# Performance work log

Measured on AMD Instinct MI355X. Metric: run time of the kernel, lower is better.

Reference implementation:

```python
import jax, jax.numpy as jnp
import numpy as np

N, G, NPG = 51200, 512, 100
E, FA, FE = 300000, 64, 8
H, NH, DH, L, T = 256, 8, 32, 4, 5


def setup_inputs() -> dict:
    key = jax.random.key(0)
    it = iter(jax.random.split(key, 40))
    def rn(shape, s=0.05):
        return jax.random.normal(next(it), shape, jnp.float32) * s
    inp = {
        "x": rn((N, FA), 1.0),
        "edge_attr": rn((E, FE), 1.0),
        "edge_index": jax.random.randint(next(it), (2, E), 0, N),
        "batch": jnp.repeat(jnp.arange(G), NPG),
        "atom_w": rn((FA, H)), "atom_b": jnp.zeros((H,), jnp.float32),
        "edge_w": rn((FE, H)), "edge_b": jnp.zeros((H,), jnp.float32),
        "gat_lin_w": rn((L, H, H)), "gat_lin_edge_w": rn((L, H, H)),
        "gat_att_src": rn((L, NH, DH)), "gat_att_dst": rn((L, NH, DH)), "gat_att_edge": rn((L, NH, DH)),
        "gat_bias": jnp.zeros((L, H), jnp.float32),
        "bn_gamma": jnp.ones((L, H), jnp.float32), "bn_beta": jnp.zeros((L, H), jnp.float32),
        "mha_in_w": rn((3 * H, H)), "mha_in_b": jnp.zeros((3 * H,), jnp.float32),
        "mha_out_w": rn((H, H)), "mha_out_b": jnp.zeros((H,), jnp.float32),
        "sh_w1": rn((H, H)), "sh_b1": jnp.zeros((H,), jnp.float32),
        "sh_w2": rn((H, H // 2)), "sh_b2": jnp.zeros((H // 2,), jnp.float32),
        "head_w1": rn((T, H // 2, H // 4)), "head_b1": jnp.zeros((T, H // 4), jnp.float32),
        "head_w2": rn((T, H // 4, 1)), "head_b2": jnp.zeros((T, 1), jnp.float32),
    }
    return inp


def _forward(x, edge_attr, edge_index, batch, atom_w, atom_b, edge_w, edge_b,
             gat_lin_w, gat_lin_edge_w, gat_att_src, gat_att_dst, gat_att_edge,
             gat_bias, bn_gamma, bn_beta, mha_in_w, mha_in_b, mha_out_w, mha_out_b,
             sh_w1, sh_b1, sh_w2, sh_b2, head_w1, head_b1, head_w2, head_b2):
    src, dst = edge_index[0], edge_index[1]
    h = x @ atom_w + atom_b                      # [N, H] atom_encoder
    e = edge_attr @ edge_w + edge_b              # [E, H] edge_encoder
    # PyG GATConv add_self_loops=True, fill_value='mean' for edge_attr
    deg = jax.ops.segment_sum(jnp.ones((E,), e.dtype), dst, num_segments=N)
    e_self = jax.ops.segment_sum(e, dst, num_segments=N) / jnp.maximum(deg, 1.0)[:, None]
    loop = jnp.arange(N)
    src_f = jnp.concatenate([src, loop])
    dst_f = jnp.concatenate([dst, loop])
    e_f = jnp.concatenate([e, e_self], axis=0)   # [E+N, H]
    for i in range(L):
        res = h
        xs = (h @ gat_lin_w[i]).reshape(N, NH, DH)
        a_src = (xs * gat_att_src[i]).sum(-1)    # [N, NH]
        a_dst = (xs * gat_att_dst[i]).sum(-1)
        ee = (e_f @ gat_lin_edge_w[i]).reshape(-1, NH, DH)
        a_e = (ee * gat_att_edge[i]).sum(-1)     # [E+N, NH]
        alpha = jax.nn.leaky_relu(a_src[src_f] + a_dst[dst_f] + a_e, 0.2)
        mx = jax.ops.segment_max(alpha, dst_f, num_segments=N)   # segment softmax over dst
        ex = jnp.exp(alpha - mx[dst_f])
        den = jax.ops.segment_sum(ex, dst_f, num_segments=N)
        w = ex / (den[dst_f] + 1e-16)            # [E+N, NH]
        out = jax.ops.segment_sum(xs[src_f] * w[..., None], dst_f, num_segments=N)
        out = out.reshape(N, H) + gat_bias[i]
        mu = out.mean(0)
        var = out.var(0)                         # training-mode BatchNorm
        out = bn_gamma[i] * (out - mu) * jax.lax.rsqrt(var + 1e-5) + bn_beta[i]
        h = jax.nn.relu(out)
        if i > 0:
            h = h + res
    # per-graph MHA: graphs are fixed-size, so the ragged loop == batched attention
    xg = h.reshape(G, NPG, H)
    qkv = xg @ mha_in_w.T + mha_in_b             # [G, n, 3H]
    q, k, v = jnp.split(qkv, 3, axis=-1)
    def heads(t):
        return t.reshape(G, NPG, NH, DH).transpose(0, 2, 1, 3)
    q = heads(q) * (1.0 / np.sqrt(DH))
    k, v = heads(k), heads(v)
    att = jax.nn.softmax(jnp.einsum("ghnd,ghmd->ghnm", q, k), axis=-1)
    o = jnp.einsum("ghnm,ghmd->ghnd", att, v).transpose(0, 2, 1, 3).reshape(G, NPG, H)
    o = o @ mha_out_w.T + mha_out_b
    pooled = o.mean(1)                           # [G, H]
    s = jax.nn.relu(pooled @ sh_w1 + sh_b1)
    s = jax.nn.relu(s @ sh_w2 + sh_b2)           # [G, H//2]
    hh = jax.nn.relu(jnp.einsum("gd,tdk->gtk", s, head_w1) + head_b1)
    pred = jnp.einsum("gtk,tko->gto", hh, head_w2)[..., 0] + head_b2[:, 0]
    return pred                                  # [G, T]


def reference(x, edge_attr, edge_index, batch, atom_w, atom_b, edge_w, edge_b,
              gat_lin_w, gat_lin_edge_w, gat_att_src, gat_att_dst, gat_att_edge,
              gat_bias, bn_gamma, bn_beta, mha_in_w, mha_in_b, mha_out_w, mha_out_b,
              sh_w1, sh_b1, sh_w2, sh_b2, head_w1, head_b1, head_w2, head_b2):
    return _forward(x, edge_attr, edge_index, batch, atom_w, atom_b, edge_w, edge_b,
                    gat_lin_w, gat_lin_edge_w, gat_att_src, gat_att_dst, gat_att_edge,
                    gat_bias, bn_gamma, bn_beta, mha_in_w, mha_in_b, mha_out_w, mha_out_b,
                    sh_w1, sh_b1, sh_w2, sh_b2, head_w1, head_b1, head_w2, head_b2)
```

## Files before the change

kernel.cpp:

```cpp
#include <hip/hip_runtime.h>
#include <hip/hip_bf16.h>

#define N_NODES 51200
#define N_EDGES 300000
#define NFULL   351200
#define GRAPHS  512
#define NPGRAPH 100
#define FATOM   64
#define FEDGE   8
#define HDIM    256
#define NHEADS  8
#define DHEAD   32
#define LAYERS  4
#define TASKS   5
#define BN_SLOTS 16

typedef unsigned short u16;
typedef __attribute__((ext_vector_type(8))) short bf16x8;
typedef __attribute__((ext_vector_type(4))) float f32x4;

__device__ __forceinline__ float b2f(u16 u) {
    return __uint_as_float(((unsigned)u) << 16);
}
__device__ __forceinline__ u16 f2bf(float f) {
    unsigned u = __float_as_uint(f);
    unsigned r = u + 0x7fffu + ((u >> 16) & 1u);
    return (u16)(r >> 16);
}

__global__ __launch_bounds__(256)
void convert_kernel(const float* __restrict__ in, u16* __restrict__ out, int n) {
    int i = blockIdx.x * 256 + threadIdx.x;
    if (i < n) out[i] = f2bf(in[i]);
}

__global__ __launch_bounds__(256)
void convert_t_kernel(const float* __restrict__ in, u16* __restrict__ out, int R, int C) {
    int idx = blockIdx.x * 256 + threadIdx.x;
    if (idx >= R * C) return;
    int c = idx / R, r = idx % R;
    out[idx] = f2bf(in[(size_t)r * C + c]);
}

template<bool BIAS, bool RELU>
__global__ __launch_bounds__(256, 2)
void gemm_mfma_kernel(const u16* __restrict__ A, const u16* __restrict__ Bt,
                      const float* __restrict__ bias, u16* __restrict__ C,
                      int M, int K, int N) {
    __shared__ u16 smem[136 * 128];
    u16* As = smem;
    u16* Bs = smem + 128 * 64;
    const int t = threadIdx.x;
    const int lane = t & 63;
    const int w = t >> 6;
    const int wr = w >> 1, wc = w & 1;

    const int nwg = (int)gridDim.x;
    const int bid = (int)blockIdx.x;
    const int q = nwg >> 3, r = nwg & 7;
    const int xcd = bid & 7, idx0 = bid >> 3;
    const int wgid = (xcd < r) ? xcd * (q + 1) + idx0
                               : r * (q + 1) + (xcd - r) * q + idx0;
    const int nx = N >> 7;
    const int bn = (wgid % nx) * 128;
    const int bm = (wgid / nx) * 128;

    f32x4 acc[4][4] = {};

    for (int kt = 0; kt < K; kt += 64) {
        uint4 ra[4], rb[4];
#pragma unroll
        for (int i = 0; i < 4; ++i) {
            int idx = i * 256 + t;
            int row = idx >> 3, ch = idx & 7;
            ra[i] = *(const uint4*)(A + (size_t)(bm + row) * K + kt + ch * 8);
            rb[i] = *(const uint4*)(Bt + (size_t)(bn + row) * K + kt + ch * 8);
        }
        __syncthreads();
#pragma unroll
        for (int i = 0; i < 4; ++i) {
            int idx = i * 256 + t;
            int row = idx >> 3, ch = idx & 7;
            int sw = ch ^ (row & 7);
            *(uint4*)((char*)As + row * 128 + sw * 16) = ra[i];
            *(uint4*)((char*)Bs + row * 128 + sw * 16) = rb[i];
        }
        __syncthreads();
#pragma unroll
        for (int kk = 0; kk < 2; ++kk) {
            bf16x8 af[4], bf[4];
#pragma unroll
            for (int m = 0; m < 4; ++m) {
                int rr = wr * 64 + m * 16 + (lane & 15);
                int ch = kk * 4 + (lane >> 4);
                af[m] = *(const bf16x8*)((const char*)As + rr * 128 + ((ch ^ (rr & 7)) << 4));
            }
#pragma unroll
            for (int n = 0; n < 4; ++n) {
                int rr = wc * 64 + n * 16 + (lane & 15);
                int ch = kk * 4 + (lane >> 4);
                bf[n] = *(const bf16x8*)((const char*)Bs + rr * 128 + ((ch ^ (rr & 7)) << 4));
            }
#pragma unroll
            for (int m = 0; m < 4; ++m)
#pragma unroll
                for (int n = 0; n < 4; ++n)
                    acc[m][n] = __builtin_amdgcn_mfma_f32_16x16x32_bf16(
                        af[m], bf[n], acc[m][n], 0, 0, 0);
        }
    }
    __syncthreads();
#pragma unroll
    for (int m = 0; m < 4; ++m)
#pragma unroll
        for (int n = 0; n < 4; ++n) {
            int coll = wc * 64 + n * 16 + (lane & 15);
            float bv = BIAS ? bias[bn + coll] : 0.f;
#pragma unroll
            for (int j = 0; j < 4; ++j) {
                float v = acc[m][n][j] + bv;
                if (RELU) v = fmaxf(v, 0.f);
                int rowl = wr * 64 + m * 16 + (lane >> 4) * 4 + j;
                smem[rowl * 136 + coll] = f2bf(v);
            }
        }
    __syncthreads();
#pragma unroll
    for (int p = 0; p < 8; ++p) {
        int rowl = p * 16 + (t >> 4);
        uint4 v = *(const uint4*)(smem + rowl * 136 + (t & 15) * 8);
        *(uint4*)(C + (size_t)(bm + rowl) * N + bn + (t & 15) * 8) = v;
    }
}

__global__ __launch_bounds__(256)
void edge_hist_kernel(const int* __restrict__ dst, int* __restrict__ deg) {
    int e = blockIdx.x * 256 + threadIdx.x;
    if (e >= N_EDGES) return;
    atomicAdd(&deg[dst[e]], 1);
}

__global__ __launch_bounds__(1024)
void scan_kernel(const int* __restrict__ deg, int* __restrict__ row_ptr) {
    __shared__ int buf[1024];
    __shared__ int carry;
    const int t = threadIdx.x;
    if (t == 0) carry = 0;
    __syncthreads();
    for (int base = 0; base < N_NODES; base += 1024) {
        int i = base + t;
        int v = deg[i] + 1;
        buf[t] = v;
        __syncthreads();
        for (int off = 1; off < 1024; off <<= 1) {
            int x = (t >= off) ? buf[t - off] : 0;
            __syncthreads();
            buf[t] += x;
            __syncthreads();
        }
        int inc = buf[t];
        int cb = carry;
        row_ptr[i] = cb + inc - v;
        __syncthreads();
        if (t == 1023) carry = cb + inc;
        __syncthreads();
    }
    if (t == 0) row_ptr[N_NODES] = carry;
}

__global__ __launch_bounds__(256)
void selfloop_init_kernel(const int* __restrict__ row_ptr, int* __restrict__ cursor,
                          int* __restrict__ col_src, int* __restrict__ col_eid) {
    int n = blockIdx.x * 256 + threadIdx.x;
    if (n >= N_NODES) return;
    cursor[n] = row_ptr[n];
    int pos = row_ptr[n + 1] - 1;
    col_src[pos] = n;
    col_eid[pos] = N_EDGES + n;
}

__global__ __launch_bounds__(256)
void scatter_kernel(const int* __restrict__ src, const int* __restrict__ dst,
                    int* __restrict__ cursor, int* __restrict__ col_src,
                    int* __restrict__ col_eid) {
    int e = blockIdx.x * 256 + threadIdx.x;
    if (e >= N_EDGES) return;
    int d = dst[e];
    int pos = atomicAdd(&cursor[d], 1);
    col_src[pos] = src[e];
    col_eid[pos] = e;
}

__global__ __launch_bounds__(256)
void proj_pe_kernel(const float* __restrict__ lin_edge_w, const float* __restrict__ att_edge,
                    float* __restrict__ P_e) {
    int idx = blockIdx.x * 256 + threadIdx.x;
    int li = idx >> 11;
    int rem = idx & 2047;
    int k = rem >> 3, nh = rem & 7;
    const float* w = lin_edge_w + (size_t)li * HDIM * HDIM + (size_t)k * HDIM + nh * DHEAD;
    const float* a = att_edge + li * HDIM + nh * DHEAD;
    float s = 0.f;
#pragma unroll
    for (int d = 0; d < DHEAD; ++d) s += w[d] * a[d];
    P_e[idx] = s;
}

__global__ __launch_bounds__(256)
void proj_q_kernel(const float* __restrict__ edge_w, const float* __restrict__ edge_b,
                   const float* __restrict__ P_e, float* __restrict__ Qm,
                   float* __restrict__ c0m) {
    int t = threadIdx.x;
    int li = t >> 6, f = (t >> 3) & 7, nh = t & 7;
    const float* pe = P_e + li * 2048;
    float q = 0.f;
    for (int k = 0; k < HDIM; ++k) q += edge_w[f * HDIM + k] * pe[k * 8 + nh];
    Qm[t] = q;
    if (t < 32) {
        int li2 = t >> 3, nh2 = t & 7;
        const float* pe2 = P_e + li2 * 2048;
        float c = 0.f;
        for (int k = 0; k < HDIM; ++k) c += edge_b[k] * pe2[k * 8 + nh2];
        c0m[t] = c;
    }
}

__global__ __launch_bounds__(256)
void ae_real_kernel(const float* __restrict__ edge_attr, const float* __restrict__ Qm,
                    const float* __restrict__ c0m, u16* __restrict__ a_e_all) {
    __shared__ float ea_s[8][8];
    __shared__ float Qs[256];
    __shared__ float c0s[32];
    const int t = threadIdx.x;
    const int e0 = blockIdx.x * 8;
    if (t < 64) ea_s[t >> 3][t & 7] = edge_attr[(size_t)e0 * 8 + t];
    Qs[t] = Qm[t];
    if (t < 32) c0s[t] = c0m[t];
    __syncthreads();
    int el = t >> 5, o = t & 31;
    int li = o >> 3, nh = o & 7;
    float v = c0s[o];
#pragma unroll
    for (int f = 0; f < 8; ++f) v += ea_s[el][f] * Qs[li * 64 + f * 8 + nh];
    a_e_all[(size_t)(e0 + el) * 32 + o] = f2bf(v);
}

__global__ __launch_bounds__(256)
void ae_self_kernel(const float* __restrict__ edge_attr, const int* __restrict__ row_ptr,
                    const int* __restrict__ col_eid, const float* __restrict__ Qm,
                    const float* __restrict__ c0m, u16* __restrict__ a_e_all) {
    __shared__ float ea_s[8][8];
    __shared__ int deg_s[8];
    __shared__ float Qs[256];
    __shared__ float c0s[32];
    const int t = threadIdx.x;
    const int n0 = blockIdx.x * 8;
    Qs[t] = Qm[t];
    if (t < 32) c0s[t] = c0m[t];
    if (t < 64) {
        int el = t >> 3, f = t & 7;
        int n = n0 + el;
        int s = row_ptr[n], e = row_ptr[n + 1] - 1;
        float acc = 0.f;
        for (int p = s; p < e; ++p)
            acc += edge_attr[(size_t)col_eid[p] * FEDGE + f];
        ea_s[el][f] = acc;
        if (f == 0) deg_s[el] = e - s;
    }
    __syncthreads();
    int el = t >> 5, o = t & 31;
    int li = o >> 3, nh = o & 7;
    int dg = deg_s[el];
    float v = 0.f;
    if (dg > 0) {
        float invd = 1.f / (float)dg;
        v = c0s[o];
#pragma unroll
        for (int f = 0; f < 8; ++f) v += ea_s[el][f] * invd * Qs[li * 64 + f * 8 + nh];
    }
    a_e_all[(size_t)(N_EDGES + n0 + el) * 32 + o] = f2bf(v);
}

__global__ __launch_bounds__(256)
void gat_asd_kernel(const u16* __restrict__ xs, const float* __restrict__ att_src_l,
                    const float* __restrict__ att_dst_l, float* __restrict__ a_src,
                    float* __restrict__ a_dst) {
    int node = (blockIdx.x << 2) + (threadIdx.x >> 6);
    int lane = threadIdx.x & 63;
    int c = lane << 2;
    ushort4 x4 = *(const ushort4*)(xs + (size_t)node * HDIM + c);
    float4 as4 = *(const float4*)(att_src_l + c);
    float4 ad4 = *(const float4*)(att_dst_l + c);
    float x0 = b2f(x4.x), x1 = b2f(x4.y), x2 = b2f(x4.z), x3 = b2f(x4.w);
    float vs = x0 * as4.x + x1 * as4.y + x2 * as4.z + x3 * as4.w;
    float vd = x0 * ad4.x + x1 * ad4.y + x2 * ad4.z + x3 * ad4.w;
#pragma unroll
    for (int off = 4; off >= 1; off >>= 1) {
        vs += __shfl_down(vs, off, 8);
        vd += __shfl_down(vd, off, 8);
    }
    if ((lane & 7) == 0) {
        a_src[node * 8 + (lane >> 3)] = vs;
        a_dst[node * 8 + (lane >> 3)] = vd;
    }
}

__global__ __launch_bounds__(256)
void gat_aggregate_kernel(const u16* __restrict__ xs, const float* __restrict__ a_src,
                          const float* __restrict__ a_dst, const u16* __restrict__ a_e_all,
                          const int* __restrict__ row_ptr, const int* __restrict__ col_src,
                          const int* __restrict__ col_eid, const float* __restrict__ bias_l,
                          u16* __restrict__ outb, int li) {
    int n = (blockIdx.x << 2) + (threadIdx.x >> 6);
    int lane = threadIdx.x & 63;
    int c = lane << 2;
    int nh = lane >> 3;
    const int aeo = li * 8 + nh;
    float adst = a_dst[n * 8 + nh];
    int s = row_ptr[n], e = row_ptr[n + 1];
    float4 acc = make_float4(0.f, 0.f, 0.f, 0.f);
    float den = 0.f;
    int p = s;
    for (; p + 4 <= e; p += 4) {
        int s0 = col_src[p],     s1 = col_src[p + 1];
        int s2 = col_src[p + 2], s3 = col_src[p + 3];
        int e0 = col_eid[p],     e1 = col_eid[p + 1];
        int e2 = col_eid[p + 2], e3 = col_eid[p + 3];
        float as0 = a_src[s0 * 8 + nh], as1 = a_src[s1 * 8 + nh];
        float as2 = a_src[s2 * 8 + nh], as3 = a_src[s3 * 8 + nh];
        float ae0 = b2f(a_e_all[(size_t)e0 * 32 + aeo]);
        float ae1 = b2f(a_e_all[(size_t)e1 * 32 + aeo]);
        float ae2 = b2f(a_e_all[(size_t)e2 * 32 + aeo]);
        float ae3 = b2f(a_e_all[(size_t)e3 * 32 + aeo]);
        ushort4 x0 = *(const ushort4*)(xs + (size_t)s0 * HDIM + c);
        ushort4 x1 = *(const ushort4*)(xs + (size_t)s1 * HDIM + c);
        ushort4 x2 = *(const ushort4*)(xs + (size_t)s2 * HDIM + c);
        ushort4 x3 = *(const ushort4*)(xs + (size_t)s3 * HDIM + c);
        float al0 = as0 + adst + ae0; al0 = (al0 > 0.f) ? al0 : 0.2f * al0;
        float al1 = as1 + adst + ae1; al1 = (al1 > 0.f) ? al1 : 0.2f * al1;
        float al2 = as2 + adst + ae2; al2 = (al2 > 0.f) ? al2 : 0.2f * al2;
        float al3 = as3 + adst + ae3; al3 = (al3 > 0.f) ? al3 : 0.2f * al3;
        float ex0 = __expf(al0), ex1 = __expf(al1);
        float ex2 = __expf(al2), ex3 = __expf(al3);
        den += (ex0 + ex1) + (ex2 + ex3);
        acc.x += ex0 * b2f(x0.x) + ex1 * b2f(x1.x) + ex2 * b2f(x2.x) + ex3 * b2f(x3.x);
        acc.y += ex0 * b2f(x0.y) + ex1 * b2f(x1.y) + ex2 * b2f(x2.y) + ex3 * b2f(x3.y);
        acc.z += ex0 * b2f(x0.z) + ex1 * b2f(x1.z) + ex2 * b2f(x2.z) + ex3 * b2f(x3.z);
        acc.w += ex0 * b2f(x0.w) + ex1 * b2f(x1.w) + ex2 * b2f(x2.w) + ex3 * b2f(x3.w);
    }
    for (; p + 2 <= e; p += 2) {
        int s0 = col_src[p],     s1 = col_src[p + 1];
        int e0 = col_eid[p],     e1 = col_eid[p + 1];
        float as0 = a_src[s0 * 8 + nh];
        float as1 = a_src[s1 * 8 + nh];
        float ae0 = b2f(a_e_all[(size_t)e0 * 32 + aeo]);
        float ae1 = b2f(a_e_all[(size_t)e1 * 32 + aeo]);
        ushort4 x0 = *(const ushort4*)(xs + (size_t)s0 * HDIM + c);
        ushort4 x1 = *(const ushort4*)(xs + (size_t)s1 * HDIM + c);
        float al0 = as0 + adst + ae0; al0 = (al0 > 0.f) ? al0 : 0.2f * al0;
        float al1 = as1 + adst + ae1; al1 = (al1 > 0.f) ? al1 : 0.2f * al1;
        float ex0 = __expf(al0);
        float ex1 = __expf(al1);
        den += ex0 + ex1;
        acc.x += ex0 * b2f(x0.x) + ex1 * b2f(x1.x);
        acc.y += ex0 * b2f(x0.y) + ex1 * b2f(x1.y);
        acc.z += ex0 * b2f(x0.z) + ex1 * b2f(x1.z);
        acc.w += ex0 * b2f(x0.w) + ex1 * b2f(x1.w);
    }
    if (p < e) {
        int s0 = col_src[p];
        int e0 = col_eid[p];
        float al = a_src[s0 * 8 + nh] + adst + b2f(a_e_all[(size_t)e0 * 32 + aeo]);
        al = (al > 0.f) ? al : 0.2f * al;
        float ex = __expf(al);
        den += ex;
        ushort4 x4 = *(const ushort4*)(xs + (size_t)s0 * HDIM + c);
        acc.x += ex * b2f(x4.x); acc.y += ex * b2f(x4.y);
        acc.z += ex * b2f(x4.z); acc.w += ex * b2f(x4.w);
    }
    float inv = 1.f / (den + 1e-16f);
    float4 b4 = *(const float4*)(bias_l + c);
    ushort4 o4;
    o4.x = f2bf(acc.x * inv + b4.x);
    o4.y = f2bf(acc.y * inv + b4.y);
    o4.z = f2bf(acc.z * inv + b4.z);
    o4.w = f2bf(acc.w * inv + b4.w);
    *(ushort4*)(outb + (size_t)n * HDIM + c) = o4;
}

__global__ __launch_bounds__(256)
void bn_stats1_kernel(const u16* __restrict__ outb, float* __restrict__ gsum,
                      float* __restrict__ gsq) {
    __shared__ float lsum[8][HDIM];
    __shared__ float lsq[8][HDIM];
    const int t = threadIdx.x;
    const int b = blockIdx.x;
    const int c0 = (t & 31) * 8;
    const int g = t >> 5;
    const size_t base = (size_t)b * 64 * HDIM;
    float s[8] = {}, q[8] = {};
#pragma unroll
    for (int i = 0; i < 8; ++i) {
        const u16* p = outb + base + i * 2048 + t * 8;
        ushort4 u0 = *(const ushort4*)p;
        ushort4 u1 = *(const ushort4*)(p + 4);
        float v0 = b2f(u0.x), v1 = b2f(u0.y), v2 = b2f(u0.z), v3 = b2f(u0.w);
        float v4 = b2f(u1.x), v5 = b2f(u1.y), v6 = b2f(u1.z), v7 = b2f(u1.w);
        s[0] += v0; q[0] += v0 * v0;  s[1] += v1; q[1] += v1 * v1;
        s[2] += v2; q[2] += v2 * v2;  s[3] += v3; q[3] += v3 * v3;
        s[4] += v4; q[4] += v4 * v4;  s[5] += v5; q[5] += v5 * v5;
        s[6] += v6; q[6] += v6 * v6;  s[7] += v7; q[7] += v7 * v7;
    }
#pragma unroll
    for (int j = 0; j < 8; ++j) { lsum[g][c0 + j] = s[j]; lsq[g][c0 + j] = q[j]; }
    __syncthreads();
    float ts = 0.f, tq = 0.f;
#pragma unroll
    for (int gg = 0; gg < 8; ++gg) { ts += lsum[gg][t]; tq += lsq[gg][t]; }
    int slot = b & (BN_SLOTS - 1);
    atomicAdd(&gsum[slot * HDIM + t], ts);
    atomicAdd(&gsq[slot * HDIM + t], tq);
}

__global__ __launch_bounds__(256)
void bn_stats2_kernel(const float* __restrict__ gsum, const float* __restrict__ gsq,
                      float* __restrict__ mu, float* __restrict__ inv) {
    int c = threadIdx.x;
    float s = 0.f, s2 = 0.f;
#pragma unroll
    for (int b = 0; b < BN_SLOTS; ++b) {
        s += gsum[b * HDIM + c];
        s2 += gsq[b * HDIM + c];
    }
    float m = s / (float)N_NODES;
    float var = s2 / (float)N_NODES - m * m;
    mu[c] = m;
    inv[c] = rsqrtf(var + 1e-5f);
}

__global__ __launch_bounds__(256)
void bn_apply_kernel(const u16* __restrict__ outb, const float* __restrict__ mu,
                     const float* __restrict__ inv, const float* __restrict__ gamma_l,
                     const float* __restrict__ beta_l, u16* __restrict__ h, int addres) {
    int idx = blockIdx.x * 256 + threadIdx.x;
    int c = (idx & 63) << 2;
    ushort4 v4 = *(const ushort4*)(outb + (size_t)idx * 4);
    float4 m4 = *(const float4*)(mu + c);
    float4 i4 = *(const float4*)(inv + c);
    float4 g4 = *(const float4*)(gamma_l + c);
    float4 b4 = *(const float4*)(beta_l + c);
    float v0 = fmaxf(g4.x * (b2f(v4.x) - m4.x) * i4.x + b4.x, 0.f);
    float v1 = fmaxf(g4.y * (b2f(v4.y) - m4.y) * i4.y + b4.y, 0.f);
    float v2 = fmaxf(g4.z * (b2f(v4.z) - m4.z) * i4.z + b4.z, 0.f);
    float v3 = fmaxf(g4.w * (b2f(v4.w) - m4.w) * i4.w + b4.w, 0.f);
    if (addres) {
        ushort4 h4 = *(const ushort4*)(h + (size_t)idx * 4);
        v0 += b2f(h4.x); v1 += b2f(h4.y); v2 += b2f(h4.z); v3 += b2f(h4.w);
    }
    ushort4 o4;
    o4.x = f2bf(v0); o4.y = f2bf(v1); o4.z = f2bf(v2); o4.w = f2bf(v3);
    *(ushort4*)(h + (size_t)idx * 4) = o4;
}

__global__ __launch_bounds__(64)
void mha_attn_kernel(const u16* __restrict__ qkv, u16* __restrict__ o) {
    const int g = blockIdx.x >> 3;
    const int head = blockIdx.x & 7;
    const int l = threadIdx.x;
    __shared__ u16 VT[DHEAD][132];
    __shared__ u16 P[16][132];
    const size_t base = (size_t)g * NPGRAPH * 768 + head * 32;

    for (int idx = l; idx < 32 * 128; idx += 64) {
        int m = idx >> 5, d = idx & 31;
        u16 v = 0;
        if (m < 100) v = qkv[base + (size_t)m * 768 + 512 + d];
        VT[d][m] = v;
    }
    bf16x8 kf[7];
#pragma unroll
    for (int n = 0; n < 7; ++n) {
        int r = n * 16 + (l & 15);
        kf[n] = *(const bf16x8*)(qkv + base + (size_t)r * 768 + 256 + ((l >> 4) << 3));
    }
    __syncthreads();
    bf16x8 vf[2][4];
#pragma unroll
    for (int dt = 0; dt < 2; ++dt)
#pragma unroll
        for (int kc = 0; kc < 4; ++kc)
            vf[dt][kc] = *(const bf16x8*)(&VT[dt * 16 + (l & 15)][kc * 32 + ((l >> 4) << 3)]);

    const float SC = 0.17677669529663687f;
    const bool c6ok = (96 + (l & 15)) < 100;

    for (int mt = 0; mt < 7; ++mt) {
        int qr = mt * 16 + (l & 15);
        bf16x8 qf = *(const bf16x8*)(qkv + base + (size_t)qr * 768 + ((l >> 4) << 3));
        f32x4 sa[7];
#pragma unroll
        for (int n = 0; n < 7; ++n) {
            f32x4 z = {0.f, 0.f, 0.f, 0.f};
            sa[n] = __builtin_amdgcn_mfma_f32_16x16x32_bf16(qf, kf[n], z, 0, 0, 0);
        }
        float linv[4];
#pragma unroll
        for (int j = 0; j < 4; ++j) {
            float m = -1e30f;
#pragma unroll
            for (int n = 0; n < 6; ++n) m = fmaxf(m, sa[n][j]);
            if (c6ok) m = fmaxf(m, sa[6][j]);
            m *= SC;
#pragma unroll
            for (int off = 1; off < 16; off <<= 1) m = fmaxf(m, __shfl_xor(m, off));
            float ls = 0.f;
            float pv[7];
#pragma unroll
            for (int n = 0; n < 7; ++n) {
                float p_ = 0.f;
                if (n < 6 || c6ok) p_ = __expf(SC * sa[n][j] - m);
                pv[n] = p_;
                ls += p_;
            }
#pragma unroll
            for (int off = 1; off < 16; off <<= 1) ls += __shfl_xor(ls, off);
            linv[j] = 1.f / ls;
            int rt = ((l >> 4) << 2) + j;
#pragma unroll
            for (int n = 0; n < 7; ++n) P[rt][n * 16 + (l & 15)] = f2bf(pv[n]);
            P[rt][112 + (l & 15)] = 0;
        }
        __syncthreads();
        f32x4 oa[2] = {};
#pragma unroll
        for (int kc = 0; kc < 4; ++kc) {
            bf16x8 pf = *(const bf16x8*)(&P[l & 15][kc * 32 + ((l >> 4) << 3)]);
            oa[0] = __builtin_amdgcn_mfma_f32_16x16x32_bf16(pf, vf[0][kc], oa[0], 0, 0, 0);
            oa[1] = __builtin_amdgcn_mfma_f32_16x16x32_bf16(pf, vf[1][kc], oa[1], 0, 0, 0);
        }
        int r0 = mt * 16 + ((l >> 4) << 2);
#pragma unroll
        for (int dt = 0; dt < 2; ++dt)
#pragma unroll
            for (int j = 0; j < 4; ++j) {
                int r = r0 + j;
                if (r < 100)
                    o[(size_t)(g * NPGRAPH + r) * HDIM + head * 32 + dt * 16 + (l & 15)] =
                        f2bf(oa[dt][j] * linv[j]);
            }
        __syncthreads();
    }
}

__global__ __launch_bounds__(256)
void pool_kernel(const u16* __restrict__ o2, u16* __restrict__ pooled) {
    int g = blockIdx.x;
    int c = threadIdx.x;
    float s = 0.f;
    for (int r = 0; r < NPGRAPH; ++r) s += b2f(o2[((size_t)g * NPGRAPH + r) * HDIM + c]);
    pooled[g * HDIM + c] = f2bf(s * 0.01f);
}

__global__ __launch_bounds__(64)
void heads_kernel(const u16* __restrict__ s2, const float* __restrict__ w1,
                  const float* __restrict__ b1, const float* __restrict__ w2,
                  const float* __restrict__ b2, float* __restrict__ out) {
    int g = blockIdx.x / TASKS;
    int tt = blockIdx.x % TASKS;
    int d = threadIdx.x;
    float s = b1[tt * 64 + d];
    const u16* srow = s2 + (size_t)g * 128;
    const float* wcol = w1 + (size_t)tt * 128 * 64 + d;
    for (int k = 0; k < 128; ++k) s += b2f(srow[k]) * wcol[k * 64];
    s = fmaxf(s, 0.f);
    float v = s * w2[tt * 64 + d];
#pragma unroll
    for (int off = 32; off >= 1; off >>= 1) v += __shfl_down(v, off);
    if (d == 0) out[g * TASKS + tt] = v + b2[tt];
}

extern "C" void kernel_launch(void* const* d_in, const int* in_sizes, int n_in,
                              void* d_out, int out_size, void* d_ws, size_t ws_size,
                              hipStream_t stream) {
    const float* x          = (const float*)d_in[0];
    const float* edge_attr  = (const float*)d_in[1];
    const int*   edge_index = (const int*)d_in[2];
    const float* atom_w     = (const float*)d_in[4];
    const float* atom_b     = (const float*)d_in[5];
    const float* edge_w     = (const float*)d_in[6];
    const float* edge_b     = (const float*)d_in[7];
    const float* gat_lin_w  = (const float*)d_in[8];
    const float* gat_lin_ew = (const float*)d_in[9];
    const float* att_src    = (const float*)d_in[10];
    const float* att_dst    = (const float*)d_in[11];
    const float* att_edge   = (const float*)d_in[12];
    const float* gat_bias   = (const float*)d_in[13];
    const float* bn_gamma   = (const float*)d_in[14];
    const float* bn_beta    = (const float*)d_in[15];
    const float* mha_in_w   = (const float*)d_in[16];
    const float* mha_in_b   = (const float*)d_in[17];
    const float* mha_out_w  = (const float*)d_in[18];
    const float* mha_out_b  = (const float*)d_in[19];
    const float* sh_w1      = (const float*)d_in[20];
    const float* sh_b1      = (const float*)d_in[21];
    const float* sh_w2      = (const float*)d_in[22];
    const float* sh_b2      = (const float*)d_in[23];
    const float* head_w1    = (const float*)d_in[24];
    const float* head_b1    = (const float*)d_in[25];
    const float* head_w2    = (const float*)d_in[26];
    const float* head_b2    = (const float*)d_in[27];
    float* out = (float*)d_out;

    const int* src = edge_index;
    const int* dst = edge_index + N_EDGES;

    size_t off = 0;
    auto alloc = [&](size_t bytes) -> void* {
        void* p = (char*)d_ws + off;
        off += (bytes + 255) & ~(size_t)255;
        return p;
    };
    const size_t NHB = (size_t)N_NODES * HDIM * sizeof(u16);
    u16* h_buf = (u16*)alloc(NHB);
    char* region1 = (char*)alloc((size_t)N_NODES * 768 * sizeof(u16));
    u16* xs_buf  = (u16*)region1;
    u16* out_buf = (u16*)(region1 + NHB);
    u16* a_e_all = (u16*)(region1 + 2 * NHB);
    u16* qkv_buf = (u16*)region1;
    u16* o2_buf  = (u16*)region1;
    u16* o_buf   = h_buf;
    u16* x_bf    = out_buf;
    float* a_src_b = (float*)alloc((size_t)N_NODES * 8 * sizeof(float));
    float* a_dst_b = (float*)alloc((size_t)N_NODES * 8 * sizeof(float));
    float* gsum    = (float*)alloc(BN_SLOTS * HDIM * sizeof(float));
    float* gsq     = (float*)alloc(BN_SLOTS * HDIM * sizeof(float));
    float* mu_b    = (float*)alloc(HDIM * sizeof(float));
    float* inv_b   = (float*)alloc(HDIM * sizeof(float));
    float* P_e     = (float*)alloc(LAYERS * HDIM * 8 * sizeof(float));
    float* Qm      = (float*)alloc(256 * sizeof(float));
    float* c0m     = (float*)alloc(32 * sizeof(float));
    u16* atom_wt   = (u16*)alloc((size_t)HDIM * FATOM * sizeof(u16));
    u16* lin_wt    = (u16*)alloc((size_t)LAYERS * HDIM * HDIM * sizeof(u16));
    u16* in_w_bf   = (u16*)alloc((size_t)768 * HDIM * sizeof(u16));
    u16* out_w_bf  = (u16*)alloc((size_t)HDIM * HDIM * sizeof(u16));
    u16* sh1_t     = (u16*)alloc((size_t)HDIM * HDIM * sizeof(u16));
    u16* sh2_t     = (u16*)alloc((size_t)128 * HDIM * sizeof(u16));
    u16* pooled    = (u16*)alloc((size_t)GRAPHS * HDIM * sizeof(u16));
    u16* s1_b      = (u16*)alloc((size_t)GRAPHS * HDIM * sizeof(u16));
    u16* s2_b      = (u16*)alloc((size_t)GRAPHS * 128 * sizeof(u16));
    int* deg       = (int*)alloc(N_NODES * sizeof(int));
    int* row_ptr   = (int*)alloc((N_NODES + 256) * sizeof(int));
    int* cursor    = (int*)alloc(N_NODES * sizeof(int));
    int* col_src   = (int*)alloc(NFULL * sizeof(int));
    int* col_eid   = (int*)alloc(NFULL * sizeof(int));
    (void)ws_size; (void)in_sizes; (void)n_in; (void)out_size;

    convert_t_kernel<<<(HDIM * FATOM + 255) / 256, 256, 0, stream>>>(atom_w, atom_wt, FATOM, HDIM);
    for (int li = 0; li < LAYERS; ++li)
        convert_t_kernel<<<(HDIM * HDIM + 255) / 256, 256, 0, stream>>>(
            gat_lin_w + (size_t)li * HDIM * HDIM, lin_wt + (size_t)li * HDIM * HDIM, HDIM, HDIM);
    convert_kernel<<<(768 * HDIM + 255) / 256, 256, 0, stream>>>(mha_in_w, in_w_bf, 768 * HDIM);
    convert_kernel<<<(HDIM * HDIM + 255) / 256, 256, 0, stream>>>(mha_out_w, out_w_bf, HDIM * HDIM);
    convert_t_kernel<<<(HDIM * HDIM + 255) / 256, 256, 0, stream>>>(sh_w1, sh1_t, HDIM, HDIM);
    convert_t_kernel<<<(HDIM * 128 + 255) / 256, 256, 0, stream>>>(sh_w2, sh2_t, HDIM, 128);
    convert_kernel<<<(N_NODES * FATOM + 255) / 256, 256, 0, stream>>>(x, x_bf, N_NODES * FATOM);

    hipMemsetAsync(deg, 0, N_NODES * sizeof(int), stream);
    edge_hist_kernel<<<(N_EDGES + 255) / 256, 256, 0, stream>>>(dst, deg);
    scan_kernel<<<1, 1024, 0, stream>>>(deg, row_ptr);
    selfloop_init_kernel<<<(N_NODES + 255) / 256, 256, 0, stream>>>(row_ptr, cursor, col_src, col_eid);
    scatter_kernel<<<(N_EDGES + 255) / 256, 256, 0, stream>>>(src, dst, cursor, col_src, col_eid);

    proj_pe_kernel<<<32, 256, 0, stream>>>(gat_lin_ew, att_edge, P_e);
    proj_q_kernel<<<1, 256, 0, stream>>>(edge_w, edge_b, P_e, Qm, c0m);
    ae_real_kernel<<<N_EDGES / 8, 256, 0, stream>>>(edge_attr, Qm, c0m, a_e_all);
    ae_self_kernel<<<N_NODES / 8, 256, 0, stream>>>(
        edge_attr, row_ptr, col_eid, Qm, c0m, a_e_all);

    gemm_mfma_kernel<true, false><<<(HDIM / 128) * (N_NODES / 128), 256, 0, stream>>>(
        x_bf, atom_wt, atom_b, h_buf, N_NODES, FATOM, HDIM);

    for (int li = 0; li < LAYERS; ++li) {
        gemm_mfma_kernel<false, false><<<(HDIM / 128) * (N_NODES / 128), 256, 0, stream>>>(
            h_buf, lin_wt + (size_t)li * HDIM * HDIM, nullptr, xs_buf, N_NODES, HDIM, HDIM);
        gat_asd_kernel<<<N_NODES / 4, 256, 0, stream>>>(
            xs_buf, att_src + li * HDIM, att_dst + li * HDIM, a_src_b, a_dst_b);
        gat_aggregate_kernel<<<N_NODES / 4, 256, 0, stream>>>(
            xs_buf, a_src_b, a_dst_b, a_e_all, row_ptr, col_src, col_eid,
            gat_bias + li * HDIM, out_buf, li);
        hipMemsetAsync(gsum, 0, BN_SLOTS * HDIM * sizeof(float), stream);
        hipMemsetAsync(gsq, 0, BN_SLOTS * HDIM * sizeof(float), stream);
        bn_stats1_kernel<<<N_NODES / 64, 256, 0, stream>>>(out_buf, gsum, gsq);
        bn_stats2_kernel<<<1, 256, 0, stream>>>(gsum, gsq, mu_b, inv_b);
        bn_apply_kernel<<<(N_NODES * HDIM / 4) / 256, 256, 0, stream>>>(
            out_buf, mu_b, inv_b, bn_gamma + li * HDIM, bn_beta + li * HDIM, h_buf, li > 0 ? 1 : 0);
    }

    gemm_mfma_kernel<true, false><<<(768 / 128) * (N_NODES / 128), 256, 0, stream>>>(
        h_buf, in_w_bf, mha_in_b, qkv_buf, N_NODES, HDIM, 768);
    mha_attn_kernel<<<GRAPHS * NHEADS, 64, 0, stream>>>(qkv_buf, o_buf);
    gemm_mfma_kernel<true, false><<<(HDIM / 128) * (N_NODES / 128), 256, 0, stream>>>(
        o_buf, out_w_bf, mha_out_b, o2_buf, N_NODES, HDIM, HDIM);
    pool_kernel<<<GRAPHS, 256, 0, stream>>>(o2_buf, pooled);

    gemm_mfma_kernel<true, true><<<(HDIM / 128) * (GRAPHS / 128), 256, 0, stream>>>(
        pooled, sh1_t, sh_b1, s1_b, GRAPHS, HDIM, HDIM);
    gemm_mfma_kernel<true, true><<<(128 / 128) * (GRAPHS / 128), 256, 0, stream>>>(
        s1_b, sh2_t, sh_b2, s2_b, GRAPHS, HDIM, 128);
    heads_kernel<<<GRAPHS * TASKS, 64, 0, stream>>>(
        s2_b, head_w1, head_b1, head_w2, head_b2, out);
}
```

Before: 965.5 us.

## Fuse QKV projection into per-graph-head MHA attention kernel

Drops the separate QKV GEMM. Each graph/head block now computes its own Q, K and V slices with MFMA straight from h and the in-projection weights, stages them in LDS, and runs attention across 4 waves instead of 1. This removes the write and re-read of the 78 MB qkv buffer and one launch, but loads the 100x256 h tile from global memory for every head without reuse. It also switches the GEMM epilogue to nontemporal stores and remaps the o/o2 buffers.

```diff
diff --git a/kernel.cpp b/kernel.cpp
--- a/kernel.cpp
+++ b/kernel.cpp
@@ -18,6 +18,7 @@
 typedef unsigned short u16;
 typedef __attribute__((ext_vector_type(8))) short bf16x8;
 typedef __attribute__((ext_vector_type(4))) float f32x4;
+typedef __attribute__((ext_vector_type(4))) unsigned int u32x4;
 
 __device__ __forceinline__ float b2f(u16 u) {
     return __uint_as_float(((unsigned)u) << 16);
@@ -128,8 +129,8 @@
 #pragma unroll
     for (int p = 0; p < 8; ++p) {
         int rowl = p * 16 + (t >> 4);
-        uint4 v = *(const uint4*)(smem + rowl * 136 + (t & 15) * 8);
-        *(uint4*)(C + (size_t)(bm + rowl) * N + bn + (t & 15) * 8) = v;
+        u32x4 v = *(const u32x4*)(smem + rowl * 136 + (t & 15) * 8);
+        __builtin_nontemporal_store(v, (u32x4*)(C + (size_t)(bm + rowl) * N + bn + (t & 15) * 8));
     }
 }
 
@@ -462,28 +463,55 @@
     *(ushort4*)(h + (size_t)idx * 4) = o4;
 }
 
-__global__ __launch_bounds__(64)
-void mha_attn_kernel(const u16* __restrict__ qkv, u16* __restrict__ o) {
+__global__ __launch_bounds__(256, 2)
+void fused_qkv_attn_kernel(const u16* __restrict__ h, const u16* __restrict__ Wb,
+                           const float* __restrict__ bias, u16* __restrict__ o) {
     const int g = blockIdx.x >> 3;
     const int head = blockIdx.x & 7;
-    const int l = threadIdx.x;
+    const int t = threadIdx.x;
+    const int l = t & 63;
+    const int w = t >> 6;
+    __shared__ u16 QL[112][36];
+    __shared__ u16 KL[112][36];
     __shared__ u16 VT[DHEAD][132];
-    __shared__ u16 P[16][132];
-    const size_t base = (size_t)g * NPGRAPH * 768 + head * 32;
-
-    for (int idx = l; idx < 32 * 128; idx += 64) {
-        int m = idx >> 5, d = idx & 31;
-        u16 v = 0;
-        if (m < 100) v = qkv[base + (size_t)m * 768 + 512 + d];
-        VT[d][m] = v;
-    }
+    __shared__ u16 P[4][16][132];
+
+    for (int idx = t; idx < 32 * 16; idx += 256)
+        VT[idx >> 4][112 + (idx & 15)] = 0;
+
+    const int hrow0 = g * NPGRAPH;
+    for (int j = w; j < 42; j += 4) {
+        int mat = j / 14, rem = j % 14;
+        int mt = rem >> 1, ntile = rem & 1;
+        int ofs = mat * 256 + head * 32;
+        int arow = hrow0 + mt * 16 + (l & 15);
+        if (arow > N_NODES - 1) arow = N_NODES - 1;
+        const u16* ap = h + (size_t)arow * HDIM + ((l >> 4) << 3);
+        const u16* bp = Wb + (size_t)(ofs + ntile * 16 + (l & 15)) * HDIM + ((l >> 4) << 3);
+        f32x4 acc = {0.f, 0.f, 0.f, 0.f};
+#pragma unroll
+        for (int ks = 0; ks < 8; ++ks)
+            acc = __builtin_amdgcn_mfma_f32_16x16x32_bf16(
+                *(const bf16x8*)(ap + ks * 32),
+                *(const bf16x8*)(bp + ks * 32), acc, 0, 0, 0);
+        int ccol = ntile * 16 + (l & 15);
+        float bv = bias[ofs + ccol];
+        int r0 = mt * 16 + ((l >> 4) << 2);
+#pragma unroll
+        for (int jj = 0; jj < 4; ++jj) {
+            int r = r0 + jj;
+            u16 val = f2bf(acc[jj] + bv);
+            if (mat == 0) QL[r][ccol] = val;
+            else if (mat == 1) KL[r][ccol] = val;
+            else VT[ccol][r] = (r < NPGRAPH) ? val : (u16)0;
+        }
+    }
+    __syncthreads();
+
     bf16x8 kf[7];
 #pragma unroll
-    for (int n = 0; n < 7; ++n) {
-        int r = n * 16 + (l & 15);
-        kf[n] = *(const bf16x8*)(qkv + base + (size_t)r * 768 + 256 + ((l >> 4) << 3));
-    }
-    __syncthreads();
+    for (int n = 0; n < 7; ++n)
+        kf[n] = *(const bf16x8*)(&KL[n * 16 + (l & 15)][(l >> 4) << 3]);
     bf16x8 vf[2][4];
 #pragma unroll
     for (int dt = 0; dt < 2; ++dt)
@@ -494,60 +522,65 @@
     const float SC = 0.17677669529663687f;
     const bool c6ok = (96 + (l & 15)) < 100;
 
-    for (int mt = 0; mt < 7; ++mt) {
-        int qr = mt * 16 + (l & 15);
-        bf16x8 qf = *(const bf16x8*)(qkv + base + (size_t)qr * 768 + ((l >> 4) << 3));
-        f32x4 sa[7];
-#pragma unroll
-        for (int n = 0; n < 7; ++n) {
-            f32x4 z = {0.f, 0.f, 0.f, 0.f};
-            sa[n] = __builtin_amdgcn_mfma_f32_16x16x32_bf16(qf, kf[n], z, 0, 0, 0);
-        }
-        float linv[4];
-#pragma unroll
-        for (int j = 0; j < 4; ++j) {
-            float m = -1e30f;
-#pragma unroll
-            for (int n = 0; n < 6; ++n) m = fmaxf(m, sa[n][j]);
-            if (c6ok) m = fmaxf(m, sa[6][j]);
-            m *= SC;
-#pragma unroll
-            for (int off = 1; off < 16; off <<= 1) m = fmaxf(m, __shfl_xor(m, off));
-            float ls = 0.f;
-            float pv[7];
+    for (int round = 0; round < 2; ++round) {
+        int mt = round * 4 + w;
+        bool active = (mt < 7);
+        float linv[4] = {1.f, 1.f, 1.f, 1.f};
+        if (active) {
+            bf16x8 qf = *(const bf16x8*)(&QL[mt * 16 + (l & 15)][(l >> 4) << 3]);
+            f32x4 sa[7];
 #pragma unroll
             for (int n = 0; n < 7; ++n) {
-                float p_ = 0.f;
-                if (n < 6 || c6ok) p_ = __expf(SC * sa[n][j] - m);
-                pv[n] = p_;
-                ls += p_;
+                f32x4 z = {0.f, 0.f, 0.f, 0.f};
+                sa[n] = __builtin_amdgcn_mfma_f32_16x16x32_bf16(qf, kf[n], z, 0, 0, 0);
             }
 #pragma unroll
-            for (int off = 1; off < 16; off <<= 1) ls += __shfl_xor(ls, off);
-            linv[j] = 1.f / ls;
-            int rt = ((l >> 4) << 2) + j;
-#pragma unroll
-            for (int n = 0; n < 7; ++n) P[rt][n * 16 + (l & 15)] = f2bf(pv[n]);
-            P[rt][112 + (l & 15)] = 0;
+            for (int jj = 0; jj < 4; ++jj) {
+                float m = -1e30f;
+#pragma unroll
+                for (int n = 0; n < 6; ++n) m = fmaxf(m, sa[n][jj]);
+                if (c6ok) m = fmaxf(m, sa[6][jj]);
+                m *= SC;
+#pragma unroll
+                for (int off2 = 1; off2 < 16; off2 <<= 1) m = fmaxf(m, __shfl_xor(m, off2));
+                float ls = 0.f;
+                float pv[7];
+#pragma unroll
+                for (int n = 0; n < 7; ++n) {
+                    float p_ = 0.f;
+                    if (n < 6 || c6ok) p_ = __expf(SC * sa[n][jj] - m);
+                    pv[n] = p_;
+                    ls += p_;
+                }
+#pragma unroll
+                for (int off2 = 1; off2 < 16; off2 <<= 1) ls += __shfl_xor(ls, off2);
+                linv[jj] = 1.f / ls;
+                int rt = ((l >> 4) << 2) + jj;
+#pragma unroll
+                for (int n = 0; n < 7; ++n) P[w][rt][n * 16 + (l & 15)] = f2bf(pv[n]);
+                P[w][rt][112 + (l & 15)] = 0;
+            }
         }
         __syncthreads();
-        f32x4 oa[2] = {};
-#pragma unroll
-        for (int kc = 0; kc < 4; ++kc) {
-            bf16x8 pf = *(const bf16x8*)(&P[l & 15][kc * 32 + ((l >> 4) << 3)]);
-            oa[0] = __builtin_amdgcn_mfma_f32_16x16x32_bf16(pf, vf[0][kc], oa[0], 0, 0, 0);
-            oa[1] = __builtin_amdgcn_mfma_f32_16x16x32_bf16(pf, vf[1][kc], oa[1], 0, 0, 0);
+        if (active) {
+            f32x4 oa[2] = {};
+#pragma unroll
+            for (int kc = 0; kc < 4; ++kc) {
+                bf16x8 pf = *(const bf16x8*)(&P[w][l & 15][kc * 32 + ((l >> 4) << 3)]);
+                oa[0] = __builtin_amdgcn_mfma_f32_16x16x32_bf16(pf, vf[0][kc], oa[0], 0, 0, 0);
+                oa[1] = __builtin_amdgcn_mfma_f32_16x16x32_bf16(pf, vf[1][kc], oa[1], 0, 0, 0);
+            }
+            int r0 = mt * 16 + ((l >> 4) << 2);
+#pragma unroll
+            for (int dt = 0; dt < 2; ++dt)
+#pragma unroll
+                for (int jj = 0; jj < 4; ++jj) {
+                    int r = r0 + jj;
+                    if (r < NPGRAPH)
+                        o[(size_t)(hrow0 + r) * HDIM + head * 32 + dt * 16 + (l & 15)] =
+                            f2bf(oa[dt][jj] * linv[jj]);
+                }
         }
-        int r0 = mt * 16 + ((l >> 4) << 2);
-#pragma unroll
-        for (int dt = 0; dt < 2; ++dt)
-#pragma unroll
-            for (int j = 0; j < 4; ++j) {
-                int r = r0 + j;
-                if (r < 100)
-                    o[(size_t)(g * NPGRAPH + r) * HDIM + head * 32 + dt * 16 + (l & 15)] =
-                        f2bf(oa[dt][j] * linv[j]);
-            }
         __syncthreads();
     }
 }
@@ -626,9 +659,8 @@
     u16* xs_buf  = (u16*)region1;
     u16* out_buf = (u16*)(region1 + NHB);
     u16* a_e_all = (u16*)(region1 + 2 * NHB);
-    u16* qkv_buf = (u16*)region1;
-    u16* o2_buf  = (u16*)region1;
-    u16* o_buf   = h_buf;
+    u16* o_buf   = (u16*)region1;
+    u16* o2_buf  = h_buf;
     u16* x_bf    = out_buf;
     float* a_src_b = (float*)alloc((size_t)N_NODES * 8 * sizeof(float));
     float* a_dst_b = (float*)alloc((size_t)N_NODES * 8 * sizeof(float));
@@ -696,9 +728,8 @@
             out_buf, mu_b, inv_b, bn_gamma + li * HDIM, bn_beta + li * HDIM, h_buf, li > 0 ? 1 : 0);
     }
 
-    gemm_mfma_kernel<true, false><<<(768 / 128) * (N_NODES / 128), 256, 0, stream>>>(
-        h_buf, in_w_bf, mha_in_b, qkv_buf, N_NODES, HDIM, 768);
-    mha_attn_kernel<<<GRAPHS * NHEADS, 64, 0, stream>>>(qkv_buf, o_buf);
+    fused_qkv_attn_kernel<<<GRAPHS * NHEADS, 256, 0, stream>>>(
+        h_buf, in_w_bf, mha_in_b, o_buf);
     gemm_mfma_kernel<true, false><<<(HDIM / 128) * (N_NODES / 128), 256, 0, stream>>>(
         o_buf, out_w_bf, mha_out_b, o2_buf, N_NODES, HDIM, HDIM);
     pool_kernel<<<GRAPHS, 256, 0, stream>>>(o2_buf, pooled);
```

After: 1.132 ms. +17.2%, slower.

## Parallelize row_ptr scan, batch layer weight transposes, and fold BN accumulator zeroing

Applied to the files above, without the earlier changes.

Replaces the single-block serial scan over 50 chunks of 1024 nodes with a three-kernel multi-block scan: per-block scan, a one-wave scan of the 50 block sums, then an offset add. The four per-layer weight transpose launches are merged into one kernel, and the per-layer memsets of the BN accumulators are replaced by zeroing inside bn_stats2 after the sums are read. The goal is to remove a long serial single-block kernel and several small launches, at the cost of two extra tiny scan launches.

```diff
diff --git a/kernel.cpp b/kernel.cpp
--- a/kernel.cpp
+++ b/kernel.cpp
@@ -14,6 +14,7 @@
 #define LAYERS  4
 #define TASKS   5
 #define BN_SLOTS 16
+#define SCAN_BLOCKS 50
 
 typedef unsigned short u16;
 typedef __attribute__((ext_vector_type(8))) short bf16x8;
@@ -40,6 +41,14 @@
     if (idx >= R * C) return;
     int c = idx / R, r = idx % R;
     out[idx] = f2bf(in[(size_t)r * C + c]);
+}
+
+__global__ __launch_bounds__(256)
+void convert_t4_kernel(const float* __restrict__ in, u16* __restrict__ out) {
+    int idx = blockIdx.x * 256 + threadIdx.x;
+    int li = idx >> 16, rem = idx & 65535;
+    int c = rem >> 8, r = rem & 255;
+    out[idx] = f2bf(in[(size_t)li * 65536 + r * 256 + c]);
 }
 
 template<bool BIAS, bool RELU>
@@ -141,31 +150,42 @@
 }
 
 __global__ __launch_bounds__(1024)
-void scan_kernel(const int* __restrict__ deg, int* __restrict__ row_ptr) {
+void scan1_kernel(const int* __restrict__ deg, int* __restrict__ row_ptr,
+                  int* __restrict__ bsum) {
     __shared__ int buf[1024];
-    __shared__ int carry;
-    const int t = threadIdx.x;
-    if (t == 0) carry = 0;
+    const int b = blockIdx.x, t = threadIdx.x;
+    const int i = b * 1024 + t;
+    int v = deg[i] + 1;
+    buf[t] = v;
     __syncthreads();
-    for (int base = 0; base < N_NODES; base += 1024) {
-        int i = base + t;
-        int v = deg[i] + 1;
-        buf[t] = v;
+    for (int off = 1; off < 1024; off <<= 1) {
+        int x = (t >= off) ? buf[t - off] : 0;
         __syncthreads();
-        for (int off = 1; off < 1024; off <<= 1) {
-            int x = (t >= off) ? buf[t - off] : 0;
-            __syncthreads();
-            buf[t] += x;
-            __syncthreads();
-        }
-        int inc = buf[t];
-        int cb = carry;
-        row_ptr[i] = cb + inc - v;
+        buf[t] += x;
         __syncthreads();
-        if (t == 1023) carry = cb + inc;
-        __syncthreads();
-    }
-    if (t == 0) row_ptr[N_NODES] = carry;
+    }
+    row_ptr[i] = buf[t] - v;
+    if (t == 1023) bsum[b] = buf[t];
+}
+
+__global__ __launch_bounds__(64)
+void scan2_kernel(int* __restrict__ bsum, int* __restrict__ row_ptr) {
+    int t = threadIdx.x;
+    int orig = (t < SCAN_BLOCKS) ? bsum[t] : 0;
+    int v = orig;
+    for (int off = 1; off < 64; off <<= 1) {
+        int x = __shfl_up(v, off);
+        if (t >= off) v += x;
+    }
+    if (t < SCAN_BLOCKS) bsum[t] = v - orig;
+    if (t == SCAN_BLOCKS - 1) row_ptr[N_NODES] = v;
+}
+
+__global__ __launch_bounds__(256)
+void scan3_kernel(int* __restrict__ row_ptr, const int* __restrict__ bsum) {
+    int i = blockIdx.x * 256 + threadIdx.x;
+    if (i >= N_NODES) return;
+    row_ptr[i] += bsum[i >> 10];
 }
 
 __global__ __launch_bounds__(256)
@@ -423,7 +443,7 @@
 }
 
 __global__ __launch_bounds__(256)
-void bn_stats2_kernel(const float* __restrict__ gsum, const float* __restrict__ gsq,
+void bn_stats2_kernel(float* __restrict__ gsum, float* __restrict__ gsq,
                       float* __restrict__ mu, float* __restrict__ inv) {
     int c = threadIdx.x;
     float s = 0.f, s2 = 0.f;
@@ -431,6 +451,8 @@
     for (int b = 0; b < BN_SLOTS; ++b) {
         s += gsum[b * HDIM + c];
         s2 += gsq[b * HDIM + c];
+        gsum[b * HDIM + c] = 0.f;
+        gsq[b * HDIM + c] = 0.f;
     }
     float m = s / (float)N_NODES;
     float var = s2 / (float)N_NODES - m * m;
@@ -653,12 +675,11 @@
     int* cursor    = (int*)alloc(N_NODES * sizeof(int));
     int* col_src   = (int*)alloc(NFULL * sizeof(int));
     int* col_eid   = (int*)alloc(NFULL * sizeof(int));
+    int* bsum      = (int*)alloc(64 * sizeof(int));
     (void)ws_size; (void)in_sizes; (void)n_in; (void)out_size;
 
     convert_t_kernel<<<(HDIM * FATOM + 255) / 256, 256, 0, stream>>>(atom_w, atom_wt, FATOM, HDIM);
-    for (int li = 0; li < LAYERS; ++li)
-        convert_t_kernel<<<(HDIM * HDIM + 255) / 256, 256, 0, stream>>>(
-            gat_lin_w + (size_t)li * HDIM * HDIM, lin_wt + (size_t)li * HDIM * HDIM, HDIM, HDIM);
+    convert_t4_kernel<<<(LAYERS * HDIM * HDIM) / 256, 256, 0, stream>>>(gat_lin_w, lin_wt);
     convert_kernel<<<(768 * HDIM + 255) / 256, 256, 0, stream>>>(mha_in_w, in_w_bf, 768 * HDIM);
     convert_kernel<<<(HDIM * HDIM + 255) / 256, 256, 0, stream>>>(mha_out_w, out_w_bf, HDIM * HDIM);
     convert_t_kernel<<<(HDIM * HDIM + 255) / 256, 256, 0, stream>>>(sh_w1, sh1_t, HDIM, HDIM);
@@ -667,7 +688,9 @@
 
     hipMemsetAsync(deg, 0, N_NODES * sizeof(int), stream);
     edge_hist_kernel<<<(N_EDGES + 255) / 256, 256, 0, stream>>>(dst, deg);
-    scan_kernel<<<1, 1024, 0, stream>>>(deg, row_ptr);
+    scan1_kernel<<<SCAN_BLOCKS, 1024, 0, stream>>>(deg, row_ptr, bsum);
+    scan2_kernel<<<1, 64, 0, stream>>>(bsum, row_ptr);
+    scan3_kernel<<<N_NODES / 256, 256, 0, stream>>>(row_ptr, bsum);
     selfloop_init_kernel<<<(N_NODES + 255) / 256, 256, 0, stream>>>(row_ptr, cursor, col_src, col_eid);
     scatter_kernel<<<(N_EDGES + 255) / 256, 256, 0, stream>>>(src, dst, cursor, col_src, col_eid);
 
@@ -680,6 +703,8 @@
     gemm_mfma_kernel<true, false><<<(HDIM / 128) * (N_NODES / 128), 256, 0, stream>>>(
         x_bf, atom_wt, atom_b, h_buf, N_NODES, FATOM, HDIM);
 
+    hipMemsetAsync(gsum, 0, BN_SLOTS * HDIM * sizeof(float), stream);
+    hipMemsetAsync(gsq, 0, BN_SLOTS * HDIM * sizeof(float), stream);
     for (int li = 0; li < LAYERS; ++li) {
         gemm_mfma_kernel<false, false><<<(HDIM / 128) * (N_NODES / 128), 256, 0, stream>>>(
             h_buf, lin_wt + (size_t)li * HDIM * HDIM, nullptr, xs_buf, N_NODES, HDIM, HDIM);
@@ -688,8 +713,6 @@
         gat_aggregate_kernel<<<N_NODES / 4, 256, 0, stream>>>(
             xs_buf, a_src_b, a_dst_b, a_e_all, row_ptr, col_src, col_eid,
             gat_bias + li * HDIM, out_buf, li);
-        hipMemsetAsync(gsum, 0, BN_SLOTS * HDIM * sizeof(float), stream);
-        hipMemsetAsync(gsq, 0, BN_SLOTS * HDIM * sizeof(float), stream);
         bn_stats1_kernel<<<N_NODES / 64, 256, 0, stream>>>(out_buf, gsum, gsq);
         bn_stats2_kernel<<<1, 256, 0, stream>>>(gsum, gsq, mu_b, inv_b);
         bn_apply_kernel<<<(N_NODES * HDIM / 4) / 256, 256, 0, stream>>>(
```

New measurement: 871.0 us (median of 2 runs). -9.8%, faster.
